# Kernel tuning notes

Measured on AMD Instinct MI355X. Metric: run time of the kernel, lower is better.

Reference implementation:

```python
import jax, jax.numpy as jnp
import numpy as np

B, L, D, KMAX = 4, 4096, 128, 16
IDX_MAX = 200000


def setup_inputs() -> dict:
    key = jax.random.key(0)
    k1, k2 = jax.random.split(key)
    # sorted integer "index" coordinate per batch element, shape [B, L, 1]
    first_index = jnp.sort(
        jax.random.randint(k1, (B, L, 1), 0, IDX_MAX, dtype=jnp.int32), axis=1
    )
    attr = jax.random.normal(k2, (B, L, D), dtype=jnp.float32)
    return {"first_index": first_index, "attr": attr}


def reference(first_index, attr):
    # first_index: [B, L, 1] int32 ; attr: [B, L, D] float32
    fi = first_index.astype(jnp.float32)  # torch code casts index to float
    c = fi[..., 0]  # [B, L] (ndims=1 coordinate)
    # full pairwise squared distance matrix [B, L, L]
    d2 = (c[:, :, None] - c[:, None, :]) ** 2
    # K nearest (smallest distance) neighbors; equivalent to argsort(d2)[..., :K]
    _, nbr = jax.lax.top_k(-d2, KMAX)  # nbr: [B, L, K] int32
    # per-batch gather of neighbor attributes -> [B, L, K, D]
    attr_nb = jax.vmap(lambda a, n: a[n])(attr, nbr)
    # neighbor index coords -> [B, L, K, 1]
    idx_nb = jax.vmap(lambda a, n: a[n])(fi, nbr)
    # |first_index - neighbor_index| -> [B, L, K, 1]
    index_distance = jnp.abs(fi[:, :, None, :] - idx_nb)
    return index_distance, attr_nb
```

## Files before the change

kernel.cpp:

```cpp
#include <hip/hip_runtime.h>

constexpr int B_ = 4;
constexpr int L_ = 4096;
constexpr int D_ = 128;
constexpr int K_ = 16;
constexpr int NKEY = 2 * K_;
constexpr int GATHER_BLOCKS = 2048;
constexpr int F4_TOTAL = B_ * L_ * K_ * (D_ / 4);
constexpr int F4_PER_BLOCK = F4_TOTAL / GATHER_BLOCKS;
constexpr int GATHER_ITERS = F4_PER_BLOCK / 256;

typedef float f32x4 __attribute__((ext_vector_type(4)));

static __device__ __forceinline__ int imin(int a, int b) { return a < b ? a : b; }
static __device__ __forceinline__ int imax(int a, int b) { return a > b ? a : b; }

__global__ __launch_bounds__(64) void nbr_search_kernel(
    const int* __restrict__ fi, int* __restrict__ keyout)
{
    const int q = blockIdx.x * 64 + threadIdx.x;
    const int b = q >> 12;
    const int i = q & (L_ - 1);
    const int* __restrict__ c = fi + b * L_;
    const int ci = c[i];

    int lo = i, hi = i;
    #pragma unroll
    for (int t = 0; t < K_ - 1; ++t) {
        int dl = (lo > 0)      ? (ci - c[lo - 1]) : 0x7FFFFFFF;
        int dr = (hi < L_ - 1) ? (c[hi + 1] - ci) : 0x7FFFFFFF;
        if (dl <= dr) --lo; else ++hi;
    }
    const int T = imax(ci - c[lo], c[hi] - ci);

    int keys[NKEY];
    #pragma unroll
    for (int t = 0; t < K_; ++t) {
        int j = lo + t;
        int v = c[j];
        int d = (v < ci) ? (ci - v) : (v - ci);
        keys[t] = (d << 12) | j;
    }

    const int vL = ci - T;
    int j0 = -1;
    if (c[lo] == vL) j0 = lo;
    else if (lo > 0 && c[lo - 1] == vL) j0 = lo - 1;
    #pragma unroll
    for (int t = 0; t < K_; ++t) keys[K_ + t] = 0x7FFFFFFF;
    if (j0 >= 0) {
        int p = j0;
        while (p > 0 && c[p - 1] == vL) --p;
        const int e = imin(lo - 1, p + (K_ - 1));
        #pragma unroll
        for (int t = 0; t < K_; ++t) {
            int j = p + t;
            if (j <= e) keys[K_ + t] = (T << 12) | j;
        }
    }

    #pragma unroll
    for (int size = 2; size <= NKEY; size <<= 1) {
        #pragma unroll
        for (int stride = size >> 1; stride > 0; stride >>= 1) {
            #pragma unroll
            for (int x = 0; x < NKEY; ++x) {
                int y = x ^ stride;
                if (y > x) {
                    bool up = ((x & size) == 0);
                    int a = keys[x], bb = keys[y];
                    int mn = imin(a, bb), mx = imax(a, bb);
                    keys[x] = up ? mn : mx;
                    keys[y] = up ? mx : mn;
                }
            }
        }
    }

    int4* ko = (int4*)(keyout + (size_t)q * K_);
    ko[0] = make_int4(keys[0],  keys[1],  keys[2],  keys[3]);
    ko[1] = make_int4(keys[4],  keys[5],  keys[6],  keys[7]);
    ko[2] = make_int4(keys[8],  keys[9],  keys[10], keys[11]);
    ko[3] = make_int4(keys[12], keys[13], keys[14], keys[15]);
}

__global__ __launch_bounds__(256) void nbr_gather_kernel(
    const float* __restrict__ attr, float* __restrict__ out_dist,
    float* __restrict__ out_attr)
{
    const int bid  = blockIdx.x;
    const int sbid = (bid & 7) * (GATHER_BLOCKS / 8) + (bid >> 3);
    const int tid  = threadIdx.x;
    const int* __restrict__ keys = (const int*)out_dist;
    const size_t base = (size_t)sbid * F4_PER_BLOCK;

    #pragma unroll 4
    for (int it = 0; it < GATHER_ITERS; ++it) {
        size_t f4 = base + (size_t)it * 256 + tid;
        int row = (int)(f4 >> 5);
        int off = (int)(f4 & 31);
        int key = keys[row];
        int j   = key & (L_ - 1);
        int bb  = row >> 16;
        const f32x4* __restrict__ src =
            (const f32x4*)attr + ((size_t)bb * L_ + j) * (D_ / 4);
        f32x4 v = src[off];
        __builtin_nontemporal_store(v, (f32x4*)out_attr + f4);
        if (off == 0)
            __builtin_nontemporal_store((float)(key >> 12), out_dist + row);
    }
}

extern "C" void kernel_launch(void* const* d_in, const int* in_sizes, int n_in,
                              void* d_out, int out_size, void* d_ws, size_t ws_size,
                              hipStream_t stream) {
    const int*   fi   = (const int*)d_in[0];
    const float* attr = (const float*)d_in[1];
    float* out      = (float*)d_out;
    float* out_dist = out;
    float* out_attr = out + (size_t)B_ * L_ * K_;

    nbr_search_kernel<<<dim3(B_ * L_ / 64), dim3(64), 0, stream>>>(
        fi, (int*)out_dist);
    nbr_gather_kernel<<<dim3(GATHER_BLOCKS), dim3(256), 0, stream>>>(
        attr, out_dist, out_attr);
}
```

Baseline: 38.72 us.

## Fuse neighbor search and attribute gather into one kernel via shared memory

Merges the search kernel and the gather kernel into a single launch. Each 256-thread block handles 8 queries: 8 threads compute the sorted neighbor keys and store the neighbor indices in shared memory, then the whole block gathers the attribute rows. This removes the second launch and the global round-trip of the keys through the output buffer. In exchange, only 8 of 256 threads do the serial search, so the other threads idle at the barrier, and the gather stores are no longer nontemporal.

```diff
diff --git a/kernel.cpp b/kernel.cpp
--- a/kernel.cpp
+++ b/kernel.cpp
@@ -1,113 +1,105 @@
 #include <hip/hip_runtime.h>
+
+typedef float f32x4 __attribute__((ext_vector_type(4)));
 
 constexpr int B_ = 4;
 constexpr int L_ = 4096;
 constexpr int D_ = 128;
 constexpr int K_ = 16;
 constexpr int NKEY = 2 * K_;
-constexpr int GATHER_BLOCKS = 2048;
-constexpr int F4_TOTAL = B_ * L_ * K_ * (D_ / 4);
-constexpr int F4_PER_BLOCK = F4_TOTAL / GATHER_BLOCKS;
-constexpr int GATHER_ITERS = F4_PER_BLOCK / 256;
-
-typedef float f32x4 __attribute__((ext_vector_type(4)));
+constexpr int QPB = 8;
+constexpr int BLOCKS = B_ * L_ / QPB;
 
 static __device__ __forceinline__ int imin(int a, int b) { return a < b ? a : b; }
 static __device__ __forceinline__ int imax(int a, int b) { return a > b ? a : b; }
 
-__global__ __launch_bounds__(64) void nbr_search_kernel(
-    const int* __restrict__ fi, int* __restrict__ keyout)
+__global__ __launch_bounds__(256) void fused_nbr_kernel(
+    const int* __restrict__ fi, const float* __restrict__ attr,
+    float* __restrict__ out_dist, float* __restrict__ out_attr)
 {
-    const int q = blockIdx.x * 64 + threadIdx.x;
-    const int b = q >> 12;
-    const int i = q & (L_ - 1);
+    __shared__ int s_nbr[QPB * K_];
+
+    const int bid  = blockIdx.x;
+    const int sbid = (bid & 7) * (BLOCKS / 8) + (bid >> 3);
+    const int q0   = sbid * QPB;
+    const int b    = q0 >> 12;
     const int* __restrict__ c = fi + b * L_;
-    const int ci = c[i];
+    const int tid = threadIdx.x;
 
-    int lo = i, hi = i;
-    #pragma unroll
-    for (int t = 0; t < K_ - 1; ++t) {
-        int dl = (lo > 0)      ? (ci - c[lo - 1]) : 0x7FFFFFFF;
-        int dr = (hi < L_ - 1) ? (c[hi + 1] - ci) : 0x7FFFFFFF;
-        if (dl <= dr) --lo; else ++hi;
-    }
-    const int T = imax(ci - c[lo], c[hi] - ci);
+    if (tid < QPB) {
+        const int i  = (q0 & (L_ - 1)) + tid;
+        const int ci = c[i];
 
-    int keys[NKEY];
-    #pragma unroll
-    for (int t = 0; t < K_; ++t) {
-        int j = lo + t;
-        int v = c[j];
-        int d = (v < ci) ? (ci - v) : (v - ci);
-        keys[t] = (d << 12) | j;
-    }
+        int lo = i, hi = i;
+        #pragma unroll
+        for (int t = 0; t < K_ - 1; ++t) {
+            int dl = (lo > 0)      ? (ci - c[lo - 1]) : 0x7FFFFFFF;
+            int dr = (hi < L_ - 1) ? (c[hi + 1] - ci) : 0x7FFFFFFF;
+            if (dl <= dr) --lo; else ++hi;
+        }
+        const int T = imax(ci - c[lo], c[hi] - ci);
 
-    const int vL = ci - T;
-    int j0 = -1;
-    if (c[lo] == vL) j0 = lo;
-    else if (lo > 0 && c[lo - 1] == vL) j0 = lo - 1;
-    #pragma unroll
-    for (int t = 0; t < K_; ++t) keys[K_ + t] = 0x7FFFFFFF;
-    if (j0 >= 0) {
-        int p = j0;
-        while (p > 0 && c[p - 1] == vL) --p;
-        const int e = imin(lo - 1, p + (K_ - 1));
+        int keys[NKEY];
         #pragma unroll
         for (int t = 0; t < K_; ++t) {
-            int j = p + t;
-            if (j <= e) keys[K_ + t] = (T << 12) | j;
+            int j = lo + t;
+            int v = c[j];
+            int d = (v < ci) ? (ci - v) : (v - ci);
+            keys[t] = (d << 12) | j;
         }
-    }
 
-    #pragma unroll
-    for (int size = 2; size <= NKEY; size <<= 1) {
+        const int vL = ci - T;
+        int j0 = -1;
+        if (c[lo] == vL) j0 = lo;
+        else if (lo > 0 && c[lo - 1] == vL) j0 = lo - 1;
         #pragma unroll
-        for (int stride = size >> 1; stride > 0; stride >>= 1) {
+        for (int t = 0; t < K_; ++t) keys[K_ + t] = 0x7FFFFFFF;
+        if (j0 >= 0) {
+            int p = j0;
+            while (p > 0 && c[p - 1] == vL) --p;
+            const int e = imin(lo - 1, p + (K_ - 1));
             #pragma unroll
-            for (int x = 0; x < NKEY; ++x) {
-                int y = x ^ stride;
-                if (y > x) {
-                    bool up = ((x & size) == 0);
-                    int a = keys[x], bb = keys[y];
-                    int mn = imin(a, bb), mx = imax(a, bb);
-                    keys[x] = up ? mn : mx;
-                    keys[y] = up ? mx : mn;
+            for (int t = 0; t < K_; ++t) {
+                int j = p + t;
+                if (j <= e) keys[K_ + t] = (T << 12) | j;
+            }
+        }
+
+        #pragma unroll
+        for (int size = 2; size <= NKEY; size <<= 1) {
+            #pragma unroll
+            for (int stride = size >> 1; stride > 0; stride >>= 1) {
+                #pragma unroll
+                for (int x = 0; x < NKEY; ++x) {
+                    int y = x ^ stride;
+                    if (y > x) {
+                        bool up = ((x & size) == 0);
+                        int a = keys[x], bb = keys[y];
+                        int mn = imin(a, bb), mx = imax(a, bb);
+                        keys[x] = up ? mn : mx;
+                        keys[y] = up ? mx : mn;
+                    }
                 }
             }
         }
+
+        float* od = out_dist + (size_t)(q0 + tid) * K_;
+        #pragma unroll
+        for (int t = 0; t < K_; ++t) {
+            s_nbr[tid * K_ + t] = keys[t] & (L_ - 1);
+            od[t] = (float)(keys[t] >> 12);
+        }
     }
+    __syncthreads();
 
-    int4* ko = (int4*)(keyout + (size_t)q * K_);
-    ko[0] = make_int4(keys[0],  keys[1],  keys[2],  keys[3]);
-    ko[1] = make_int4(keys[4],  keys[5],  keys[6],  keys[7]);
-    ko[2] = make_int4(keys[8],  keys[9],  keys[10], keys[11]);
-    ko[3] = make_int4(keys[12], keys[13], keys[14], keys[15]);
-}
-
-__global__ __launch_bounds__(256) void nbr_gather_kernel(
-    const float* __restrict__ attr, float* __restrict__ out_dist,
-    float* __restrict__ out_attr)
-{
-    const int bid  = blockIdx.x;
-    const int sbid = (bid & 7) * (GATHER_BLOCKS / 8) + (bid >> 3);
-    const int tid  = threadIdx.x;
-    const int* __restrict__ keys = (const int*)out_dist;
-    const size_t base = (size_t)sbid * F4_PER_BLOCK;
-
-    #pragma unroll 4
-    for (int it = 0; it < GATHER_ITERS; ++it) {
-        size_t f4 = base + (size_t)it * 256 + tid;
-        int row = (int)(f4 >> 5);
-        int off = (int)(f4 & 31);
-        int key = keys[row];
-        int j   = key & (L_ - 1);
-        int bb  = row >> 16;
-        const f32x4* __restrict__ src =
-            (const f32x4*)attr + ((size_t)bb * L_ + j) * (D_ / 4);
-        f32x4 v = src[off];
-        __builtin_nontemporal_store(v, (f32x4*)out_attr + f4);
-        if (off == 0)
-            __builtin_nontemporal_store((float)(key >> 12), out_dist + row);
+    const f32x4* __restrict__ ab = (const f32x4*)(attr + (size_t)b * L_ * D_);
+    f32x4* __restrict__ dst = (f32x4*)out_attr + (size_t)q0 * (K_ * D_ / 4);
+    const int lane = tid & 31, grp = tid >> 5;
+    #pragma unroll 8
+    for (int it = 0; it < 16; ++it) {
+        int row = it * 8 + grp;
+        int j = s_nbr[row];
+        dst[(size_t)row * 32 + lane] = ab[(size_t)j * 32 + lane];
     }
 }
 
@@ -120,8 +112,6 @@
     float* out_dist = out;
     float* out_attr = out + (size_t)B_ * L_ * K_;
 
-    nbr_search_kernel<<<dim3(B_ * L_ / 64), dim3(64), 0, stream>>>(
-        fi, (int*)out_dist);
-    nbr_gather_kernel<<<dim3(GATHER_BLOCKS), dim3(256), 0, stream>>>(
-        attr, out_dist, out_attr);
+    fused_nbr_kernel<<<dim3(BLOCKS), dim3(256), 0, stream>>>(
+        fi, attr, out_dist, out_attr);
 }
```

Measured after the change: 32.21 us. 1.2x faster.
